# Kernel tuning notes

Hardware: AMD Instinct MI355X
Metric: run time of the kernel (lower is better)

## Reference

```python
import jax, jax.numpy as jnp
import numpy as np

NUM_OBJ_CLS = 151  # Visual Genome object classes


def setup_inputs() -> dict:
    key = jax.random.key(0)
    ks = jax.random.split(key, 10)
    N_OBJ, HIDDEN, POOL, N_REL, N_RELCLS = 8192, 512, 4096, 32768, 51
    s = lambda d: 1.0 / np.sqrt(d)
    return {
        "edge_ctx": jax.random.normal(ks[0], (N_OBJ, HIDDEN), jnp.float32),
        "rel_pair_idx": jax.random.randint(ks[1], (N_REL, 2), 0, N_OBJ, jnp.int64),
        "union_features": jax.random.normal(ks[2], (N_REL, POOL), jnp.float32),
        "W_obj": jax.random.normal(ks[3], (HIDDEN, NUM_OBJ_CLS), jnp.float32) * s(HIDDEN),
        "b_obj": jnp.zeros((NUM_OBJ_CLS,), jnp.float32),
        "W_post_emb": jax.random.normal(ks[4], (HIDDEN, 2 * HIDDEN), jnp.float32) * s(HIDDEN),
        "b_post_emb": jnp.zeros((2 * HIDDEN,), jnp.float32),
        "W_post_cat": jax.random.normal(ks[5], (2 * HIDDEN, POOL), jnp.float32) * s(2 * HIDDEN),
        "b_post_cat": jnp.zeros((POOL,), jnp.float32),
        "W_rel": jax.random.normal(ks[6], (POOL, N_RELCLS), jnp.float32) * s(POOL),
        "b_rel": jnp.zeros((N_RELCLS,), jnp.float32),
        "freq_bias": jax.random.normal(ks[7], (NUM_OBJ_CLS * NUM_OBJ_CLS, N_RELCLS), jnp.float32),
    }


def reference(edge_ctx, rel_pair_idx, union_features, W_obj, b_obj,
              W_post_emb, b_post_emb, W_post_cat, b_post_cat, W_rel, b_rel,
              freq_bias):
    hidden = edge_ctx.shape[-1]
    # object classifier (stand-in for context layer's obj head)
    obj_dists = edge_ctx @ W_obj + b_obj                       # [N_obj, 151]
    obj_preds = jnp.argmax(obj_dists, axis=-1)                 # [N_obj]
    # post_emb -> split into head / tail representations
    edge_rep = (edge_ctx @ W_post_emb + b_post_emb).reshape(-1, 2, hidden)
    head_rep = edge_rep[:, 0]                                  # [N_obj, hidden]
    tail_rep = edge_rep[:, 1]
    # gather pair reps (global indices == per-image split + local gather + cat)
    h_idx, t_idx = rel_pair_idx[:, 0], rel_pair_idx[:, 1]
    prod_rep = jnp.concatenate([head_rep[h_idx], tail_rep[t_idx]], axis=-1)  # [N_rel, 2*hidden]
    prod_rep = prod_rep @ W_post_cat + b_post_cat              # [N_rel, pool]
    prod_rep = prod_rep * union_features                       # use_vision
    rel_dists = prod_rep @ W_rel + b_rel                       # [N_rel, 51]
    # frequency bias lookup on predicted (head, tail) label pairs
    pair_lbl = obj_preds[h_idx] * NUM_OBJ_CLS + obj_preds[t_idx]
    rel_dists = rel_dists + freq_bias[pair_lbl]
    return rel_dists
```

## Files before the change

### kernel.cpp

```cpp
#include <hip/hip_runtime.h>
#include <hip/hip_bf16.h>
#include <hip/hip_fp16.h>

typedef _Float16 f16;
typedef _Float16 f16x8 __attribute__((ext_vector_type(8)));
typedef _Float16 f16x4 __attribute__((ext_vector_type(4)));
typedef float f32x4 __attribute__((ext_vector_type(4)));

#define N_OBJ 8192
#define HIDDEN 512
#define POOL 4096
#define N_REL 32768
#define N_RELCLS 51
#define NUM_OBJ_CLS 151

#define WS_E16    0UL
#define WS_WPE16  8388608UL
#define WS_WCATT  9437184UL
#define WS_FT     17825792UL
#define WS_P      26214400UL
#define WS_BIAS   160432128UL
#define WS_PREDS  160448512UL
#define WS_WFRAG  160481280UL

typedef const __attribute__((address_space(1))) void* gas_ptr;
typedef __attribute__((address_space(3))) void* las_ptr;
__device__ __forceinline__ void gl_lds16(const f16* g, f16* l) {
    __builtin_amdgcn_global_load_lds((gas_ptr)g, (las_ptr)l, 16, 0, 0);
}

__global__ __launch_bounds__(256) void k_prep(const float* __restrict__ edge_ctx, const float* __restrict__ Wpe,
                                              const float* __restrict__ Wcat, const float* __restrict__ bpe,
                                              const float* __restrict__ bcat, const float* __restrict__ Wrel,
                                              f16* __restrict__ E16, f16* __restrict__ Wpe16,
                                              f16* __restrict__ WcatT, float* __restrict__ bias,
                                              f16* __restrict__ wfrag) {
    __shared__ float tile[32][33];
    __shared__ float red[8][32];
    int bid = blockIdx.x, tid = threadIdx.x;
    if (bid < 1024) {
        const f32x4* in = (const f32x4*)edge_ctx;
        f16x4* out = (f16x4*)E16;
        int base = bid * 1024 + tid;
        #pragma unroll
        for (int s = 0; s < 4; s++) {
            f32x4 v = in[base + s * 256];
            f16x4 h; h[0]=(f16)v[0]; h[1]=(f16)v[1]; h[2]=(f16)v[2]; h[3]=(f16)v[3];
            out[base + s * 256] = h;
        }
    } else if (bid < 1152) {
        const f32x4* in = (const f32x4*)Wpe;
        f16x4* out = (f16x4*)Wpe16;
        int base = (bid - 1024) * 1024 + tid;
        #pragma unroll
        for (int s = 0; s < 4; s++) {
            f32x4 v = in[base + s * 256];
            f16x4 h; h[0]=(f16)v[0]; h[1]=(f16)v[1]; h[2]=(f16)v[2]; h[3]=(f16)v[3];
            out[base + s * 256] = h;
        }
    } else if (bid < 5248) {
        int t = bid - 1152;
        int c0 = (t & 127) * 32, r0 = (t >> 7) * 32;
        int tx = tid & 31, ty = tid >> 5;
        #pragma unroll
        for (int i = 0; i < 4; i++)
            tile[ty + 8 * i][tx] = Wcat[(size_t)(r0 + ty + 8 * i) * POOL + c0 + tx];
        __syncthreads();
        #pragma unroll
        for (int i = 0; i < 4; i++)
            WcatT[(size_t)(c0 + ty + 8 * i) * (2 * HIDDEN) + r0 + tx] = (f16)tile[tx][ty + 8 * i];
    } else if (bid < 5376) {
        int c = (bid - 5248) * 32 + (tid & 31);
        int jq = tid >> 5;
        float acc = 0.0f;
        #pragma unroll 4
        for (int j = jq * 128; j < jq * 128 + 128; j++)
            acc += bpe[j] * Wcat[(size_t)j * POOL + c];
        red[jq][tid & 31] = acc;
        __syncthreads();
        if (jq == 0) {
            float s = bcat[c];
            #pragma unroll
            for (int q = 0; q < 8; q++) s += red[q][tid & 31];
            bias[c] = s;
        }
    } else {
        int kstep = bid - 5376;
        int lane = tid & 63;
        int nt = tid >> 6;
        int n = nt * 16 + (lane & 15);
        int k0 = kstep * 32 + (lane >> 4) * 8;
        f16x8 v;
        #pragma unroll
        for (int jj = 0; jj < 8; jj++) {
            float w = (n < N_RELCLS) ? Wrel[(size_t)(k0 + jj) * N_RELCLS + n] : 0.0f;
            v[jj] = (f16)w;
        }
        ((f16x8*)wfrag)[(size_t)(kstep * 4 + nt) * 64 + lane] = v;
    }
}

#define OPB 8
__global__ __launch_bounds__(256) void k_argmax(const float* __restrict__ E, const float* __restrict__ Wobj,
                                                const float* __restrict__ bobj, int* __restrict__ preds) {
    __shared__ float se[OPB * HIDDEN];
    __shared__ double part[2][OPB][5][32];
    __shared__ double redv[OPB][32];
    __shared__ int    redj[OPB][32];
    int tid = threadIdx.x;
    int o0 = blockIdx.x * OPB;
    const f32x4* Ev = (const f32x4*)(E + (size_t)o0 * HIDDEN);
    f32x4* sev = (f32x4*)se;
    #pragma unroll
    for (int i = 0; i < OPB * HIDDEN / 4 / 256; i++)
        sev[tid + i * 256] = Ev[tid + i * 256];
    __syncthreads();

    int ks = tid >> 5;
    int jg = tid & 31;
    int jgc = (jg < 31) ? jg : 30;
    double acc[OPB][5];
    #pragma unroll
    for (int o = 0; o < OPB; o++)
        #pragma unroll
        for (int jj = 0; jj < 5; jj++) acc[o][jj] = 0.0;

    int kbase = ks * 64;
    for (int k4 = 0; k4 < 16; k4++) {
        int k = kbase + k4 * 4;
        f32x4 ev[OPB];
        #pragma unroll
        for (int o = 0; o < OPB; o++) ev[o] = *(const f32x4*)(se + o * HIDDEN + k);
        #pragma unroll
        for (int kk = 0; kk < 4; kk++) {
            const float* wrow = Wobj + (size_t)(k + kk) * NUM_OBJ_CLS;
            float wv[5];
            #pragma unroll
            for (int jj = 0; jj < 5; jj++) {
                int j = jj * 31 + jgc;
                wv[jj] = wrow[(j < NUM_OBJ_CLS) ? j : (NUM_OBJ_CLS - 1)];
            }
            #pragma unroll
            for (int o = 0; o < OPB; o++) {
                double e = (double)ev[o][kk];
                #pragma unroll
                for (int jj = 0; jj < 5; jj++)
                    acc[o][jj] = fma(e, (double)wv[jj], acc[o][jj]);
            }
        }
    }

    #pragma unroll
    for (int o = 0; o < OPB; o++)
        #pragma unroll
        for (int jj = 0; jj < 5; jj++)
            acc[o][jj] += __shfl_xor(acc[o][jj], 32);
    int w = tid >> 6, lane = tid & 63;
    if (w >= 2 && lane < 32) {
        #pragma unroll
        for (int o = 0; o < OPB; o++)
            #pragma unroll
            for (int jj = 0; jj < 5; jj++) part[w - 2][o][jj][lane] = acc[o][jj];
    }
    __syncthreads();
    if (w < 2 && lane < 32) {
        #pragma unroll
        for (int o = 0; o < OPB; o++)
            #pragma unroll
            for (int jj = 0; jj < 5; jj++) acc[o][jj] += part[w][o][jj][lane];
    }
    __syncthreads();
    if (w == 1 && lane < 32) {
        #pragma unroll
        for (int o = 0; o < OPB; o++)
            #pragma unroll
            for (int jj = 0; jj < 5; jj++) part[0][o][jj][lane] = acc[o][jj];
    }
    __syncthreads();
    if (w == 0 && lane < 31) {
        #pragma unroll
        for (int o = 0; o < OPB; o++) {
            double best = -1e300; int bj = NUM_OBJ_CLS;
            #pragma unroll
            for (int jj = 0; jj < 5; jj++) {
                int j = jj * 31 + lane;
                if (j < NUM_OBJ_CLS) {
                    double v = acc[o][jj] + part[0][o][jj][lane] + (double)bobj[j];
                    if (v > best || (v == best && j < bj)) { best = v; bj = j; }
                }
            }
            redv[o][lane] = best; redj[o][lane] = bj;
        }
    }
    __syncthreads();
    if (tid < OPB) {
        int o = tid;
        double best = -1e300; int bj = NUM_OBJ_CLS;
        for (int g = 0; g < 31; g++) {
            double v = redv[o][g]; int j = redj[o][g];
            if (v > best || (v == best && j < bj)) { best = v; bj = j; }
        }
        preds[o0 + o] = bj;
    }
}

template<bool SPLITM>
__global__ __launch_bounds__(256) void k_gemm(const f16* __restrict__ A, const f16* __restrict__ B,
                                              f16* __restrict__ C, const float* __restrict__ bias,
                                              int K, int lda, int ldb, int ldc,
                                              long aZ, long bZ, long cZ, int biasLimit) {
    __shared__ f16 As[2][128 * 32];
    __shared__ f16 Bs[2][128 * 32];
    long z = blockIdx.z;
    A += z * aZ; B += z * bZ; C += z * cZ;

    int tid = threadIdx.x;
    int w = tid >> 6, lane = tid & 63;
    int wm = w >> 1, wn = w & 1;
    int lr = lane & 15, lg = lane >> 4;
    int mBase = blockIdx.y * 128;
    int nBase = blockIdx.x * 128;

    const f16* aSrc[2]; const f16* bSrc[2];
    f16* aDst[2]; f16* bDst[2];
    #pragma unroll
    for (int p = 0; p < 2; p++) {
        int c = p * 256 + tid;
        int row = c >> 2, slot = c & 3;
        int g = (slot ^ ((row ^ (row >> 2)) & 3)) * 8;
        aSrc[p] = A + (size_t)(mBase + row) * lda + g;
        bSrc[p] = B + (size_t)(nBase + row) * ldb + g;
        aDst[p] = As[0] + p * 2048 + w * 512;
        bDst[p] = Bs[0] + p * 2048 + w * 512;
    }
    int swzL = ((lr & 3) ^ ((lr >> 2) & 3)) * 8;
    f32x4 acc[4][4] = {};
    int nt = K >> 5;

    #pragma unroll
    for (int p = 0; p < 2; p++) { gl_lds16(aSrc[p], aDst[p]); gl_lds16(bSrc[p], bDst[p]); }

    for (int t = 0; t < nt; t++) {
        __syncthreads();
        int cur = t & 1;
        if (t + 1 < nt) {
            int koff = (t + 1) * 32;
            int nxt = (cur ^ 1) * 4096;
            #pragma unroll
            for (int p = 0; p < 2; p++) {
                gl_lds16(aSrc[p] + koff, aDst[p] + nxt);
                gl_lds16(bSrc[p] + koff, bDst[p] + nxt);
            }
        }
        const f16* Ab = As[cur];
        const f16* Bb = Bs[cur];
        f16x8 av[4], bv[4];
        #pragma unroll
        for (int i = 0; i < 4; i++) {
            av[i] = *(const f16x8*)(Ab + (wm * 64 + i * 16 + lr) * 32 + ((lg * 8) ^ swzL));
            bv[i] = *(const f16x8*)(Bb + (wn * 64 + i * 16 + lr) * 32 + ((lg * 8) ^ swzL));
        }
        #pragma unroll
        for (int i = 0; i < 4; i++)
            #pragma unroll
            for (int jj = 0; jj < 4; jj++)
                acc[i][jj] = __builtin_amdgcn_mfma_f32_16x16x32_f16(av[i], bv[jj], acc[i][jj], 0, 0, 0);
    }

    #pragma unroll
    for (int i = 0; i < 4; i++) {
        int mb = mBase + wm * 64 + i * 16 + lg * 4;
        f32x4 bi = {};
        if (bias && mb < biasLimit) bi = *(const f32x4*)(bias + mb);
        #pragma unroll
        for (int jj = 0; jj < 4; jj++) {
            int n = nBase + wn * 64 + jj * 16 + lr;
            f16x4 hv;
            #pragma unroll
            for (int r = 0; r < 4; r++) hv[r] = (f16)(acc[i][jj][r] + bi[r]);
            if (SPLITM) {
                size_t off = ((size_t)((mb >= POOL) ? N_OBJ : 0) + n) * POOL + (mb & (POOL - 1));
                *(f16x4*)(C + off) = hv;
            } else {
                *(f16x4*)(C + (size_t)n * ldc + mb) = hv;
            }
        }
    }
}

__global__ __launch_bounds__(256) void k_final(const f16* __restrict__ P, const float* __restrict__ U,
                                               const int* __restrict__ relp, const int* __restrict__ preds,
                                               const f16* __restrict__ wfrag, const float* __restrict__ brel,
                                               const float* __restrict__ fbias, float* __restrict__ out) {
    int w = threadIdx.x >> 6;
    int lane = threadIdx.x & 63;
    int lr = lane & 15, lg = lane >> 4;
    int r0 = blockIdx.x * 64 + w * 16;
    int arow = r0 + lr;
    int h = relp[2 * arow], t = relp[2 * arow + 1];
    const f16* ph = P + (size_t)h * POOL;
    const f16* pt = P + (size_t)(N_OBJ + t) * POOL;
    const float* u = U + (size_t)arow * POOL;
    f32x4 acc[4] = {};
    for (int ks = 0; ks < POOL / 32; ks++) {
        int ka = ks * 32 + lg * 8;
        f16x8 vh = *(const f16x8*)(ph + ka);
        f16x8 vt = *(const f16x8*)(pt + ka);
        f32x4 u0 = __builtin_nontemporal_load((const f32x4*)(u + ka));
        f32x4 u1 = __builtin_nontemporal_load((const f32x4*)(u + ka + 4));
        f16x8 a;
        #pragma unroll
        for (int jj = 0; jj < 8; jj++) {
            float uu = (jj < 4) ? u0[jj] : u1[jj - 4];
            a[jj] = (f16)(((float)vh[jj] + (float)vt[jj]) * uu);
        }
        const f16x8* bf = (const f16x8*)wfrag + (size_t)ks * 4 * 64 + lane;
        #pragma unroll
        for (int nt = 0; nt < 4; nt++)
            acc[nt] = __builtin_amdgcn_mfma_f32_16x16x32_f16(a, bf[nt * 64], acc[nt], 0, 0, 0);
    }
    #pragma unroll
    for (int r = 0; r < 4; r++) {
        int row = r0 + lg * 4 + r;
        int h2 = relp[2 * row], t2 = relp[2 * row + 1];
        int lbl = preds[h2] * NUM_OBJ_CLS + preds[t2];
        const float* fb = fbias + (size_t)lbl * N_RELCLS;
        #pragma unroll
        for (int nt = 0; nt < 4; nt++) {
            int j = nt * 16 + lr;
            if (j < N_RELCLS)
                out[(size_t)row * N_RELCLS + j] = acc[nt][r] + brel[j] + fb[j];
        }
    }
}

extern "C" void kernel_launch(void* const* d_in, const int* in_sizes, int n_in,
                              void* d_out, int out_size, void* d_ws, size_t ws_size,
                              hipStream_t stream) {
    const float* edge_ctx = (const float*)d_in[0];
    const int*   relp     = (const int*)d_in[1];
    const float* U        = (const float*)d_in[2];
    const float* Wobj     = (const float*)d_in[3];
    const float* bobj     = (const float*)d_in[4];
    const float* Wpe      = (const float*)d_in[5];
    const float* bpe      = (const float*)d_in[6];
    const float* Wcat     = (const float*)d_in[7];
    const float* bcat     = (const float*)d_in[8];
    const float* Wrel     = (const float*)d_in[9];
    const float* brel     = (const float*)d_in[10];
    const float* fbias    = (const float*)d_in[11];
    float* out = (float*)d_out;

    char* ws = (char*)d_ws;
    f16*   E16    = (f16*)(ws + WS_E16);
    f16*   Wpe16  = (f16*)(ws + WS_WPE16);
    f16*   WcatT  = (f16*)(ws + WS_WCATT);
    f16*   FT     = (f16*)(ws + WS_FT);
    f16*   P      = (f16*)(ws + WS_P);
    float* bias   = (float*)(ws + WS_BIAS);
    int*   preds  = (int*)(ws + WS_PREDS);
    f16*   wfrag  = (f16*)(ws + WS_WFRAG);

    k_prep<<<5504, 256, 0, stream>>>(edge_ctx, Wpe, Wcat, bpe, bcat, Wrel,
                                     E16, Wpe16, WcatT, bias, wfrag);
    k_argmax<<<N_OBJ / OPB, 256, 0, stream>>>(edge_ctx, Wobj, bobj, preds);
    k_gemm<false><<<dim3(POOL / 128, HIDDEN / 128, 2), 256, 0, stream>>>(
        Wpe16, WcatT, FT, nullptr, HIDDEN, 2 * HIDDEN, 2 * HIDDEN, HIDDEN,
        512L, 512L, (long)POOL * HIDDEN, 0);
    k_gemm<true><<<dim3(N_OBJ / 128, (2 * POOL) / 128, 1), 256, 0, stream>>>(
        FT, E16, P, bias, HIDDEN, HIDDEN, HIDDEN, POOL,
        0L, 0L, 0L, POOL);
    k_final<<<N_REL / 64, 256, 0, stream>>>(P, U, relp, preds, wfrag, brel, fbias, out);
}
```

Measured before the change: 387.0 us.

## Deepen GEMM K-tile with explicit vmcnt pipelining, XCD swizzle, prefetch in final kernel

The GEMM kernel now stages 64-wide K tiles with a new XOR swizzle, issues two stages ahead, and uses explicit s_waitcnt vmcnt plus raw barriers instead of __syncthreads. It also remaps workgroup IDs in an 8-way interleave so neighbouring tiles land together. The final kernel software-pipelines its global loads of P, U and weight fragments one iteration ahead of the MFMA work. The aim is to hide global memory latency and cut barrier overhead, at the cost of more LDS and registers per block, which may lower occupancy.

```diff
diff --git a/kernel.cpp b/kernel.cpp
--- a/kernel.cpp
+++ b/kernel.cpp
@@ -209,62 +209,84 @@
                                               f16* __restrict__ C, const float* __restrict__ bias,
                                               int K, int lda, int ldb, int ldc,
                                               long aZ, long bZ, long cZ, int biasLimit) {
-    __shared__ f16 As[2][128 * 32];
-    __shared__ f16 Bs[2][128 * 32];
+    __shared__ f16 As[2][128 * 64];
+    __shared__ f16 Bs[2][128 * 64];
     long z = blockIdx.z;
     A += z * aZ; B += z * bZ; C += z * cZ;
+
+    int nwg = gridDim.x * gridDim.y;
+    int wg  = blockIdx.y * gridDim.x + blockIdx.x;
+    int qq  = nwg >> 3;
+    int sw  = (wg & 7) * qq + (wg >> 3);
+    int bx  = sw % gridDim.x, by = sw / gridDim.x;
 
     int tid = threadIdx.x;
     int w = tid >> 6, lane = tid & 63;
     int wm = w >> 1, wn = w & 1;
     int lr = lane & 15, lg = lane >> 4;
-    int mBase = blockIdx.y * 128;
-    int nBase = blockIdx.x * 128;
-
-    const f16* aSrc[2]; const f16* bSrc[2];
-    f16* aDst[2]; f16* bDst[2];
-    #pragma unroll
-    for (int p = 0; p < 2; p++) {
+    int mBase = by * 128;
+    int nBase = bx * 128;
+
+    const f16* aSrc[4]; const f16* bSrc[4];
+    int dstOff[4];
+    #pragma unroll
+    for (int p = 0; p < 4; p++) {
         int c = p * 256 + tid;
-        int row = c >> 2, slot = c & 3;
-        int g = (slot ^ ((row ^ (row >> 2)) & 3)) * 8;
-        aSrc[p] = A + (size_t)(mBase + row) * lda + g;
-        bSrc[p] = B + (size_t)(nBase + row) * ldb + g;
-        aDst[p] = As[0] + p * 2048 + w * 512;
-        bDst[p] = Bs[0] + p * 2048 + w * 512;
-    }
-    int swzL = ((lr & 3) ^ ((lr >> 2) & 3)) * 8;
+        int row = c >> 3, slot = c & 7;
+        int scol = (slot ^ (row & 7)) * 8;
+        aSrc[p] = A + (size_t)(mBase + row) * lda + scol;
+        bSrc[p] = B + (size_t)(nBase + row) * ldb + scol;
+        dstOff[p] = p * 2048 + w * 512;
+    }
+    int swz = (lr & 7) << 4;
     f32x4 acc[4][4] = {};
-    int nt = K >> 5;
-
-    #pragma unroll
-    for (int p = 0; p < 2; p++) { gl_lds16(aSrc[p], aDst[p]); gl_lds16(bSrc[p], bDst[p]); }
-
-    for (int t = 0; t < nt; t++) {
-        __syncthreads();
+    int NT = K >> 6;
+
+    auto stage = [&](int t, int buf) {
+        int k0 = t * 64;
+        #pragma unroll
+        for (int p = 0; p < 4; p++) {
+            gl_lds16(aSrc[p] + k0, &As[buf][dstOff[p]]);
+            gl_lds16(bSrc[p] + k0, &Bs[buf][dstOff[p]]);
+        }
+    };
+
+    stage(0, 0);
+    if (NT > 1) stage(1, 1);
+
+    for (int t = 0; t < NT; t++) {
         int cur = t & 1;
-        if (t + 1 < nt) {
-            int koff = (t + 1) * 32;
-            int nxt = (cur ^ 1) * 4096;
-            #pragma unroll
-            for (int p = 0; p < 2; p++) {
-                gl_lds16(aSrc[p] + koff, aDst[p] + nxt);
-                gl_lds16(bSrc[p] + koff, bDst[p] + nxt);
+        if (t < NT - 1) {
+            asm volatile("s_waitcnt vmcnt(8)" ::: "memory");
+        } else {
+            asm volatile("s_waitcnt vmcnt(0)" ::: "memory");
+        }
+        __builtin_amdgcn_sched_barrier(0);
+        __builtin_amdgcn_s_barrier();
+        __builtin_amdgcn_sched_barrier(0);
+
+        f16x8 av[2][4], bv[2][4];
+        #pragma unroll
+        for (int kh = 0; kh < 2; kh++) {
+            int koff = ((kh * 64 + lg * 16) ^ swz) >> 1;
+            #pragma unroll
+            for (int i = 0; i < 4; i++) {
+                av[kh][i] = *(const f16x8*)(&As[cur][(wm * 64 + i * 16 + lr) * 64 + koff]);
+                bv[kh][i] = *(const f16x8*)(&Bs[cur][(wn * 64 + i * 16 + lr) * 64 + koff]);
             }
         }
-        const f16* Ab = As[cur];
-        const f16* Bb = Bs[cur];
-        f16x8 av[4], bv[4];
-        #pragma unroll
-        for (int i = 0; i < 4; i++) {
-            av[i] = *(const f16x8*)(Ab + (wm * 64 + i * 16 + lr) * 32 + ((lg * 8) ^ swzL));
-            bv[i] = *(const f16x8*)(Bb + (wn * 64 + i * 16 + lr) * 32 + ((lg * 8) ^ swzL));
-        }
-        #pragma unroll
-        for (int i = 0; i < 4; i++)
-            #pragma unroll
-            for (int jj = 0; jj < 4; jj++)
-                acc[i][jj] = __builtin_amdgcn_mfma_f32_16x16x32_f16(av[i], bv[jj], acc[i][jj], 0, 0, 0);
+        #pragma unroll
+        for (int kh = 0; kh < 2; kh++)
+            #pragma unroll
+            for (int i = 0; i < 4; i++)
+                #pragma unroll
+                for (int jj = 0; jj < 4; jj++)
+                    acc[i][jj] = __builtin_amdgcn_mfma_f32_16x16x32_f16(av[kh][i], bv[kh][jj], acc[i][jj], 0, 0, 0);
+
+        __builtin_amdgcn_sched_barrier(0);
+        __builtin_amdgcn_s_barrier();
+        __builtin_amdgcn_sched_barrier(0);
+        if (t + 2 < NT) stage(t + 2, cur);
     }
 
     #pragma unroll
@@ -301,23 +323,38 @@
     const f16* ph = P + (size_t)h * POOL;
     const f16* pt = P + (size_t)(N_OBJ + t) * POOL;
     const float* u = U + (size_t)arow * POOL;
+    const f16x8* bfb = (const f16x8*)wfrag + lane;
+
+    int ka0 = lg * 8;
+    f16x8 vh = *(const f16x8*)(ph + ka0);
+    f16x8 vt = *(const f16x8*)(pt + ka0);
+    f32x4 u0 = __builtin_nontemporal_load((const f32x4*)(u + ka0));
+    f32x4 u1 = __builtin_nontemporal_load((const f32x4*)(u + ka0 + 4));
+    f16x8 b0 = bfb[0], b1 = bfb[64], b2 = bfb[128], b3 = bfb[192];
+
     f32x4 acc[4] = {};
     for (int ks = 0; ks < POOL / 32; ks++) {
-        int ka = ks * 32 + lg * 8;
-        f16x8 vh = *(const f16x8*)(ph + ka);
-        f16x8 vt = *(const f16x8*)(pt + ka);
-        f32x4 u0 = __builtin_nontemporal_load((const f32x4*)(u + ka));
-        f32x4 u1 = __builtin_nontemporal_load((const f32x4*)(u + ka + 4));
+        f16x8 cvh = vh, cvt = vt, cb0 = b0, cb1 = b1, cb2 = b2, cb3 = b3;
+        f32x4 cu0 = u0, cu1 = u1;
+        if (ks + 1 < POOL / 32) {
+            int ka = (ks + 1) * 32 + lg * 8;
+            vh = *(const f16x8*)(ph + ka);
+            vt = *(const f16x8*)(pt + ka);
+            u0 = __builtin_nontemporal_load((const f32x4*)(u + ka));
+            u1 = __builtin_nontemporal_load((const f32x4*)(u + ka + 4));
+            const f16x8* bf = bfb + (size_t)(ks + 1) * 256;
+            b0 = bf[0]; b1 = bf[64]; b2 = bf[128]; b3 = bf[192];
+        }
         f16x8 a;
         #pragma unroll
         for (int jj = 0; jj < 8; jj++) {
-            float uu = (jj < 4) ? u0[jj] : u1[jj - 4];
-            a[jj] = (f16)(((float)vh[jj] + (float)vt[jj]) * uu);
-        }
-        const f16x8* bf = (const f16x8*)wfrag + (size_t)ks * 4 * 64 + lane;
-        #pragma unroll
-        for (int nt = 0; nt < 4; nt++)
-            acc[nt] = __builtin_amdgcn_mfma_f32_16x16x32_f16(a, bf[nt * 64], acc[nt], 0, 0, 0);
+            float uu = (jj < 4) ? cu0[jj] : cu1[jj - 4];
+            a[jj] = (f16)(((float)cvh[jj] + (float)cvt[jj]) * uu);
+        }
+        acc[0] = __builtin_amdgcn_mfma_f32_16x16x32_f16(a, cb0, acc[0], 0, 0, 0);
+        acc[1] = __builtin_amdgcn_mfma_f32_16x16x32_f16(a, cb1, acc[1], 0, 0, 0);
+        acc[2] = __builtin_amdgcn_mfma_f32_16x16x32_f16(a, cb2, acc[2], 0, 0, 0);
+        acc[3] = __builtin_amdgcn_mfma_f32_16x16x32_f16(a, cb3, acc[3], 0, 0, 0);
     }
     #pragma unroll
     for (int r = 0; r < 4; r++) {
```

Result: slower. 446.4 us (+15.3%).

## Use 256x256 GEMM tiles with deeper prefetch and fold argmax into prep kernel

Applied to the files above, without the earlier changes.

The GEMM kernel now uses 256x256 output tiles with a K step of 64, 512 threads, and a two-stage global-to-LDS prefetch. It waits on explicit vmcnt counts and raises wave priority around the MFMA section. Workgroup indices are remapped so that neighbouring tiles share operands in cache. The object argmax kernel is merged into the prep kernel as extra blocks, which removes one launch and lets it overlap with the weight conversions. The trade-off is a larger LDS footprint (128 KB per block), higher register pressure, and fewer blocks for the smaller GEMM.

```diff
diff --git a/kernel.cpp b/kernel.cpp
--- a/kernel.cpp
+++ b/kernel.cpp
@@ -29,37 +29,135 @@
     __builtin_amdgcn_global_load_lds((gas_ptr)g, (las_ptr)l, 16, 0, 0);
 }
 
+#define OPB 8
 __global__ __launch_bounds__(256) void k_prep(const float* __restrict__ edge_ctx, const float* __restrict__ Wpe,
                                               const float* __restrict__ Wcat, const float* __restrict__ bpe,
                                               const float* __restrict__ bcat, const float* __restrict__ Wrel,
+                                              const float* __restrict__ Wobj, const float* __restrict__ bobj,
                                               f16* __restrict__ E16, f16* __restrict__ Wpe16,
                                               f16* __restrict__ WcatT, float* __restrict__ bias,
-                                              f16* __restrict__ wfrag) {
+                                              f16* __restrict__ wfrag, int* __restrict__ preds) {
+    __shared__ float se[OPB * HIDDEN];
+    __shared__ double part[2][OPB][5][32];
+    __shared__ double redv[OPB][32];
+    __shared__ int    redj[OPB][32];
     __shared__ float tile[32][33];
     __shared__ float red[8][32];
     int bid = blockIdx.x, tid = threadIdx.x;
     if (bid < 1024) {
+        int o0 = bid * OPB;
+        const f32x4* Ev = (const f32x4*)(edge_ctx + (size_t)o0 * HIDDEN);
+        f32x4* sev = (f32x4*)se;
+        #pragma unroll
+        for (int i = 0; i < OPB * HIDDEN / 4 / 256; i++)
+            sev[tid + i * 256] = Ev[tid + i * 256];
+        __syncthreads();
+        int ks = tid >> 5;
+        int jg = tid & 31;
+        int jgc = (jg < 31) ? jg : 30;
+        double acc[OPB][5];
+        #pragma unroll
+        for (int o = 0; o < OPB; o++)
+            #pragma unroll
+            for (int jj = 0; jj < 5; jj++) acc[o][jj] = 0.0;
+        int kbase = ks * 64;
+        for (int k4 = 0; k4 < 16; k4++) {
+            int k = kbase + k4 * 4;
+            f32x4 ev[OPB];
+            #pragma unroll
+            for (int o = 0; o < OPB; o++) ev[o] = *(const f32x4*)(se + o * HIDDEN + k);
+            #pragma unroll
+            for (int kk = 0; kk < 4; kk++) {
+                const float* wrow = Wobj + (size_t)(k + kk) * NUM_OBJ_CLS;
+                float wv[5];
+                #pragma unroll
+                for (int jj = 0; jj < 5; jj++) {
+                    int j = jj * 31 + jgc;
+                    wv[jj] = wrow[(j < NUM_OBJ_CLS) ? j : (NUM_OBJ_CLS - 1)];
+                }
+                #pragma unroll
+                for (int o = 0; o < OPB; o++) {
+                    double e = (double)ev[o][kk];
+                    #pragma unroll
+                    for (int jj = 0; jj < 5; jj++)
+                        acc[o][jj] = fma(e, (double)wv[jj], acc[o][jj]);
+                }
+            }
+        }
+        #pragma unroll
+        for (int o = 0; o < OPB; o++)
+            #pragma unroll
+            for (int jj = 0; jj < 5; jj++)
+                acc[o][jj] += __shfl_xor(acc[o][jj], 32);
+        int w = tid >> 6, lane = tid & 63;
+        if (w >= 2 && lane < 32) {
+            #pragma unroll
+            for (int o = 0; o < OPB; o++)
+                #pragma unroll
+                for (int jj = 0; jj < 5; jj++) part[w - 2][o][jj][lane] = acc[o][jj];
+        }
+        __syncthreads();
+        if (w < 2 && lane < 32) {
+            #pragma unroll
+            for (int o = 0; o < OPB; o++)
+                #pragma unroll
+                for (int jj = 0; jj < 5; jj++) acc[o][jj] += part[w][o][jj][lane];
+        }
+        __syncthreads();
+        if (w == 1 && lane < 32) {
+            #pragma unroll
+            for (int o = 0; o < OPB; o++)
+                #pragma unroll
+                for (int jj = 0; jj < 5; jj++) part[0][o][jj][lane] = acc[o][jj];
+        }
+        __syncthreads();
+        if (w == 0 && lane < 31) {
+            #pragma unroll
+            for (int o = 0; o < OPB; o++) {
+                double best = -1e300; int bj = NUM_OBJ_CLS;
+                #pragma unroll
+                for (int jj = 0; jj < 5; jj++) {
+                    int j = jj * 31 + lane;
+                    if (j < NUM_OBJ_CLS) {
+                        double v = acc[o][jj] + part[0][o][jj][lane] + (double)bobj[j];
+                        if (v > best || (v == best && j < bj)) { best = v; bj = j; }
+                    }
+                }
+                redv[o][lane] = best; redj[o][lane] = bj;
+            }
+        }
+        __syncthreads();
+        if (tid < OPB) {
+            int o = tid;
+            double best = -1e300; int bj = NUM_OBJ_CLS;
+            for (int g = 0; g < 31; g++) {
+                double v = redv[o][g]; int j = redj[o][g];
+                if (v > best || (v == best && j < bj)) { best = v; bj = j; }
+            }
+            preds[o0 + o] = bj;
+        }
+    } else if (bid < 2048) {
         const f32x4* in = (const f32x4*)edge_ctx;
         f16x4* out = (f16x4*)E16;
-        int base = bid * 1024 + tid;
+        int base = (bid - 1024) * 1024 + tid;
         #pragma unroll
         for (int s = 0; s < 4; s++) {
             f32x4 v = in[base + s * 256];
             f16x4 h; h[0]=(f16)v[0]; h[1]=(f16)v[1]; h[2]=(f16)v[2]; h[3]=(f16)v[3];
             out[base + s * 256] = h;
         }
-    } else if (bid < 1152) {
+    } else if (bid < 2176) {
         const f32x4* in = (const f32x4*)Wpe;
         f16x4* out = (f16x4*)Wpe16;
-        int base = (bid - 1024) * 1024 + tid;
+        int base = (bid - 2048) * 1024 + tid;
         #pragma unroll
         for (int s = 0; s < 4; s++) {
             f32x4 v = in[base + s * 256];
             f16x4 h; h[0]=(f16)v[0]; h[1]=(f16)v[1]; h[2]=(f16)v[2]; h[3]=(f16)v[3];
             out[base + s * 256] = h;
         }
-    } else if (bid < 5248) {
-        int t = bid - 1152;
+    } else if (bid < 6272) {
+        int t = bid - 2176;
         int c0 = (t & 127) * 32, r0 = (t >> 7) * 32;
         int tx = tid & 31, ty = tid >> 5;
         #pragma unroll
@@ -69,8 +167,8 @@
         #pragma unroll
         for (int i = 0; i < 4; i++)
             WcatT[(size_t)(c0 + ty + 8 * i) * (2 * HIDDEN) + r0 + tx] = (f16)tile[tx][ty + 8 * i];
-    } else if (bid < 5376) {
-        int c = (bid - 5248) * 32 + (tid & 31);
+    } else if (bid < 6400) {
+        int c = (bid - 6272) * 32 + (tid & 31);
         int jq = tid >> 5;
         float acc = 0.0f;
         #pragma unroll 4
@@ -85,7 +183,7 @@
             bias[c] = s;
         }
     } else {
-        int kstep = bid - 5376;
+        int kstep = bid - 6400;
         int lane = tid & 63;
         int nt = tid >> 6;
         int n = nt * 16 + (lane & 15);
@@ -100,184 +198,112 @@
     }
 }
 
-#define OPB 8
-__global__ __launch_bounds__(256) void k_argmax(const float* __restrict__ E, const float* __restrict__ Wobj,
-                                                const float* __restrict__ bobj, int* __restrict__ preds) {
-    __shared__ float se[OPB * HIDDEN];
-    __shared__ double part[2][OPB][5][32];
-    __shared__ double redv[OPB][32];
-    __shared__ int    redj[OPB][32];
-    int tid = threadIdx.x;
-    int o0 = blockIdx.x * OPB;
-    const f32x4* Ev = (const f32x4*)(E + (size_t)o0 * HIDDEN);
-    f32x4* sev = (f32x4*)se;
-    #pragma unroll
-    for (int i = 0; i < OPB * HIDDEN / 4 / 256; i++)
-        sev[tid + i * 256] = Ev[tid + i * 256];
-    __syncthreads();
-
-    int ks = tid >> 5;
-    int jg = tid & 31;
-    int jgc = (jg < 31) ? jg : 30;
-    double acc[OPB][5];
-    #pragma unroll
-    for (int o = 0; o < OPB; o++)
-        #pragma unroll
-        for (int jj = 0; jj < 5; jj++) acc[o][jj] = 0.0;
-
-    int kbase = ks * 64;
-    for (int k4 = 0; k4 < 16; k4++) {
-        int k = kbase + k4 * 4;
-        f32x4 ev[OPB];
-        #pragma unroll
-        for (int o = 0; o < OPB; o++) ev[o] = *(const f32x4*)(se + o * HIDDEN + k);
-        #pragma unroll
-        for (int kk = 0; kk < 4; kk++) {
-            const float* wrow = Wobj + (size_t)(k + kk) * NUM_OBJ_CLS;
-            float wv[5];
-            #pragma unroll
-            for (int jj = 0; jj < 5; jj++) {
-                int j = jj * 31 + jgc;
-                wv[jj] = wrow[(j < NUM_OBJ_CLS) ? j : (NUM_OBJ_CLS - 1)];
-            }
-            #pragma unroll
-            for (int o = 0; o < OPB; o++) {
-                double e = (double)ev[o][kk];
-                #pragma unroll
-                for (int jj = 0; jj < 5; jj++)
-                    acc[o][jj] = fma(e, (double)wv[jj], acc[o][jj]);
-            }
-        }
-    }
-
-    #pragma unroll
-    for (int o = 0; o < OPB; o++)
-        #pragma unroll
-        for (int jj = 0; jj < 5; jj++)
-            acc[o][jj] += __shfl_xor(acc[o][jj], 32);
-    int w = tid >> 6, lane = tid & 63;
-    if (w >= 2 && lane < 32) {
-        #pragma unroll
-        for (int o = 0; o < OPB; o++)
-            #pragma unroll
-            for (int jj = 0; jj < 5; jj++) part[w - 2][o][jj][lane] = acc[o][jj];
-    }
-    __syncthreads();
-    if (w < 2 && lane < 32) {
-        #pragma unroll
-        for (int o = 0; o < OPB; o++)
-            #pragma unroll
-            for (int jj = 0; jj < 5; jj++) acc[o][jj] += part[w][o][jj][lane];
-    }
-    __syncthreads();
-    if (w == 1 && lane < 32) {
-        #pragma unroll
-        for (int o = 0; o < OPB; o++)
-            #pragma unroll
-            for (int jj = 0; jj < 5; jj++) part[0][o][jj][lane] = acc[o][jj];
-    }
-    __syncthreads();
-    if (w == 0 && lane < 31) {
-        #pragma unroll
-        for (int o = 0; o < OPB; o++) {
-            double best = -1e300; int bj = NUM_OBJ_CLS;
-            #pragma unroll
-            for (int jj = 0; jj < 5; jj++) {
-                int j = jj * 31 + lane;
-                if (j < NUM_OBJ_CLS) {
-                    double v = acc[o][jj] + part[0][o][jj][lane] + (double)bobj[j];
-                    if (v > best || (v == best && j < bj)) { best = v; bj = j; }
-                }
-            }
-            redv[o][lane] = best; redj[o][lane] = bj;
-        }
-    }
-    __syncthreads();
-    if (tid < OPB) {
-        int o = tid;
-        double best = -1e300; int bj = NUM_OBJ_CLS;
-        for (int g = 0; g < 31; g++) {
-            double v = redv[o][g]; int j = redj[o][g];
-            if (v > best || (v == best && j < bj)) { best = v; bj = j; }
-        }
-        preds[o0 + o] = bj;
-    }
-}
-
 template<bool SPLITM>
-__global__ __launch_bounds__(256) void k_gemm(const f16* __restrict__ A, const f16* __restrict__ B,
-                                              f16* __restrict__ C, const float* __restrict__ bias,
-                                              int K, int lda, int ldb, int ldc,
-                                              long aZ, long bZ, long cZ, int biasLimit) {
-    __shared__ f16 As[2][128 * 32];
-    __shared__ f16 Bs[2][128 * 32];
+__global__ __launch_bounds__(512, 2) void k_gemm256(const f16* __restrict__ A, const f16* __restrict__ B,
+                                                    f16* __restrict__ C, const float* __restrict__ bias,
+                                                    int K, int lda, int ldb, int ldc,
+                                                    long aZ, long bZ, long cZ, int biasLimit) {
+    __shared__ f16 As[2][256 * 64];
+    __shared__ f16 Bs[2][256 * 64];
     long z = blockIdx.z;
     A += z * aZ; B += z * bZ; C += z * cZ;
 
+    int nwg = gridDim.x * gridDim.y;
+    int wg  = blockIdx.y * gridDim.x + blockIdx.x;
+    int q   = nwg >> 3;
+    int sw  = (wg & 7) * q + (wg >> 3);
+    int bx  = sw % gridDim.x, by = sw / gridDim.x;
+    int mBase = by * 256, nBase = bx * 256;
+
     int tid = threadIdx.x;
-    int w = tid >> 6, lane = tid & 63;
-    int wm = w >> 1, wn = w & 1;
+    int wid = tid >> 6, lane = tid & 63;
+    int wm = wid >> 2, wn = wid & 3;
     int lr = lane & 15, lg = lane >> 4;
-    int mBase = blockIdx.y * 128;
-    int nBase = blockIdx.x * 128;
-
-    const f16* aSrc[2]; const f16* bSrc[2];
-    f16* aDst[2]; f16* bDst[2];
+
+    const f16* aS[4]; const f16* bS[4]; int dOff[4];
     #pragma unroll
-    for (int p = 0; p < 2; p++) {
-        int c = p * 256 + tid;
-        int row = c >> 2, slot = c & 3;
-        int g = (slot ^ ((row ^ (row >> 2)) & 3)) * 8;
-        aSrc[p] = A + (size_t)(mBase + row) * lda + g;
-        bSrc[p] = B + (size_t)(nBase + row) * ldb + g;
-        aDst[p] = As[0] + p * 2048 + w * 512;
-        bDst[p] = Bs[0] + p * 2048 + w * 512;
-    }
-    int swzL = ((lr & 3) ^ ((lr >> 2) & 3)) * 8;
-    f32x4 acc[4][4] = {};
-    int nt = K >> 5;
+    for (int l = 0; l < 4; l++) {
+        int c = l * 512 + tid;
+        int row = c >> 3, slot = c & 7;
+        int gcol = (slot ^ (row & 7)) * 8;
+        aS[l] = A + (size_t)(mBase + row) * lda + gcol;
+        bS[l] = B + (size_t)(nBase + row) * ldb + gcol;
+        dOff[l] = l * 4096 + wid * 512;
+    }
+
+    f32x4 acc[8][4] = {};
+    int NT = K >> 6;
+    int lrs = lr & 7;
 
     #pragma unroll
-    for (int p = 0; p < 2; p++) { gl_lds16(aSrc[p], aDst[p]); gl_lds16(bSrc[p], bDst[p]); }
-
-    for (int t = 0; t < nt; t++) {
-        __syncthreads();
+    for (int l = 0; l < 4; l++) { gl_lds16(aS[l], &As[0][dOff[l]]); gl_lds16(bS[l], &Bs[0][dOff[l]]); }
+    if (NT > 1) {
+        #pragma unroll
+        for (int l = 0; l < 4; l++) { gl_lds16(aS[l] + 64, &As[1][dOff[l]]); gl_lds16(bS[l] + 64, &Bs[1][dOff[l]]); }
+    }
+
+    for (int t = 0; t < NT; t++) {
         int cur = t & 1;
-        if (t + 1 < nt) {
-            int koff = (t + 1) * 32;
-            int nxt = (cur ^ 1) * 4096;
-            #pragma unroll
-            for (int p = 0; p < 2; p++) {
-                gl_lds16(aSrc[p] + koff, aDst[p] + nxt);
-                gl_lds16(bSrc[p] + koff, bDst[p] + nxt);
-            }
-        }
+        if (t + 1 < NT) { asm volatile("s_waitcnt vmcnt(8)" ::: "memory"); }
+        else            { asm volatile("s_waitcnt vmcnt(0)" ::: "memory"); }
+        __builtin_amdgcn_sched_barrier(0);
+        __builtin_amdgcn_s_barrier();
+
         const f16* Ab = As[cur];
         const f16* Bb = Bs[cur];
-        f16x8 av[4], bv[4];
-        #pragma unroll
-        for (int i = 0; i < 4; i++) {
-            av[i] = *(const f16x8*)(Ab + (wm * 64 + i * 16 + lr) * 32 + ((lg * 8) ^ swzL));
-            bv[i] = *(const f16x8*)(Bb + (wn * 64 + i * 16 + lr) * 32 + ((lg * 8) ^ swzL));
-        }
-        #pragma unroll
-        for (int i = 0; i < 4; i++)
-            #pragma unroll
-            for (int jj = 0; jj < 4; jj++)
-                acc[i][jj] = __builtin_amdgcn_mfma_f32_16x16x32_f16(av[i], bv[jj], acc[i][jj], 0, 0, 0);
+        #pragma unroll
+        for (int p = 0; p < 4; p++) {
+            int mh = p & 1, nh = p >> 1;
+            f16x8 a[4][2], b[2][2];
+            #pragma unroll
+            for (int ks = 0; ks < 2; ks++) {
+                int slotb = ks * 4 + lg;
+                #pragma unroll
+                for (int mf = 0; mf < 4; mf++) {
+                    int row = wm * 128 + mh * 64 + mf * 16 + lr;
+                    a[mf][ks] = *(const f16x8*)(Ab + row * 64 + ((slotb ^ lrs) * 8));
+                }
+                #pragma unroll
+                for (int nf = 0; nf < 2; nf++) {
+                    int row = wn * 64 + nh * 32 + nf * 16 + lr;
+                    b[nf][ks] = *(const f16x8*)(Bb + row * 64 + ((slotb ^ lrs) * 8));
+                }
+            }
+            __builtin_amdgcn_s_setprio(1);
+            #pragma unroll
+            for (int ks = 0; ks < 2; ks++)
+                #pragma unroll
+                for (int mf = 0; mf < 4; mf++)
+                    #pragma unroll
+                    for (int nf = 0; nf < 2; nf++)
+                        acc[mh * 4 + mf][nh * 2 + nf] =
+                            __builtin_amdgcn_mfma_f32_16x16x32_f16(a[mf][ks], b[nf][ks],
+                                                                   acc[mh * 4 + mf][nh * 2 + nf], 0, 0, 0);
+            __builtin_amdgcn_s_setprio(0);
+            __builtin_amdgcn_sched_barrier(0);
+        }
+        __builtin_amdgcn_s_barrier();
+        if (t + 2 < NT) {
+            int k0 = (t + 2) * 64;
+            #pragma unroll
+            for (int l = 0; l < 4; l++) {
+                gl_lds16(aS[l] + k0, &As[cur][dOff[l]]);
+                gl_lds16(bS[l] + k0, &Bs[cur][dOff[l]]);
+            }
+        }
     }
 
     #pragma unroll
-    for (int i = 0; i < 4; i++) {
-        int mb = mBase + wm * 64 + i * 16 + lg * 4;
+    for (int ai = 0; ai < 8; ai++) {
+        int mb = mBase + wm * 128 + ai * 16 + lg * 4;
         f32x4 bi = {};
         if (bias && mb < biasLimit) bi = *(const f32x4*)(bias + mb);
         #pragma unroll
-        for (int jj = 0; jj < 4; jj++) {
-            int n = nBase + wn * 64 + jj * 16 + lr;
+        for (int bj = 0; bj < 4; bj++) {
+            int n = nBase + wn * 64 + bj * 16 + lr;
             f16x4 hv;
             #pragma unroll
-            for (int r = 0; r < 4; r++) hv[r] = (f16)(acc[i][jj][r] + bi[r]);
+            for (int r = 0; r < 4; r++) hv[r] = (f16)(acc[ai][bj][r] + bi[r]);
             if (SPLITM) {
                 size_t off = ((size_t)((mb >= POOL) ? N_OBJ : 0) + n) * POOL + (mb & (POOL - 1));
                 *(f16x4*)(C + off) = hv;
@@ -361,13 +387,12 @@
     int*   preds  = (int*)(ws + WS_PREDS);
     f16*   wfrag  = (f16*)(ws + WS_WFRAG);
 
-    k_prep<<<5504, 256, 0, stream>>>(edge_ctx, Wpe, Wcat, bpe, bcat, Wrel,
-                                     E16, Wpe16, WcatT, bias, wfrag);
-    k_argmax<<<N_OBJ / OPB, 256, 0, stream>>>(edge_ctx, Wobj, bobj, preds);
-    k_gemm<false><<<dim3(POOL / 128, HIDDEN / 128, 2), 256, 0, stream>>>(
+    k_prep<<<6528, 256, 0, stream>>>(edge_ctx, Wpe, Wcat, bpe, bcat, Wrel, Wobj, bobj,
+                                     E16, Wpe16, WcatT, bias, wfrag, preds);
+    k_gemm256<false><<<dim3(POOL / 256, HIDDEN / 256, 2), 512, 0, stream>>>(
         Wpe16, WcatT, FT, nullptr, HIDDEN, 2 * HIDDEN, 2 * HIDDEN, HIDDEN,
         512L, 512L, (long)POOL * HIDDEN, 0);
-    k_gemm<true><<<dim3(N_OBJ / 128, (2 * POOL) / 128, 1), 256, 0, stream>>>(
+    k_gemm256<true><<<dim3(N_OBJ / 256, (2 * POOL) / 256, 1), 512, 0, stream>>>(
         FT, E16, P, bias, HIDDEN, HIDDEN, HIDDEN, POOL,
         0L, 0L, 0L, POOL);
     k_final<<<N_REL / 64, 256, 0, stream>>>(P, U, relp, preds, wfrag, brel, fbias, out);
```

Result: slower. 425.5 us (+9.9%).
